# Optimization experiments

Measured on AMD Instinct MI355X. Metric: run time of the kernel, lower is better.

## Reference

```python
import jax, jax.numpy as jnp
import numpy as np

N_NODES = 50000
N_EDGES = 800000
MUL = 32            # multiplicity of 0e and 1o feature irreps
N_SPECIES = 4       # node_attr = 4x0e one-hot
N_BASIS = 8         # radial basis scalars
N_HID = 8           # invariant_neurons
AVG_NEIGH = 16.0
INV_SQRT3 = 1.0 / np.sqrt(3.0).astype(np.float32)


def setup_inputs() -> dict:
    key = jax.random.key(0)
    ks = jax.random.split(key, 16)
    x = jax.random.normal(ks[0], (N_NODES, MUL * 4), jnp.float32)  # 32x0e + 32x1o
    species = jax.random.randint(ks[1], (N_NODES,), 0, N_SPECIES)
    node_attr = jax.nn.one_hot(species, N_SPECIES, dtype=jnp.float32)
    edge_embedding = jax.random.normal(ks[2], (N_EDGES, N_BASIS), jnp.float32)
    edge_attr = jax.random.normal(ks[3], (N_EDGES, 4), jnp.float32)  # 1x0e + 1x1o
    edge_index = jax.random.randint(ks[4], (2, N_EDGES), 0, N_NODES)
    # learned params
    W_lin1_s = jax.random.normal(ks[5], (MUL, MUL), jnp.float32)
    W_lin1_v = jax.random.normal(ks[6], (MUL, MUL), jnp.float32)
    fc_w1 = jax.random.normal(ks[7], (N_BASIS, N_HID), jnp.float32)
    fc_w2 = jax.random.normal(ks[8], (N_HID, 4 * MUL), jnp.float32)  # tp.weight_numel = 4*MUL
    W_lin2_s = jax.random.normal(ks[9], (2 * MUL, MUL), jnp.float32)  # mid simplify: 64x0e
    W_lin2_v = jax.random.normal(ks[10], (2 * MUL, MUL), jnp.float32)  # 64x1o
    W_sc_s = jax.random.normal(ks[11], (MUL, N_SPECIES, MUL), jnp.float32)
    W_sc_v = jax.random.normal(ks[12], (MUL, N_SPECIES, MUL), jnp.float32)
    return dict(node_features=x, node_attr=node_attr, edge_embedding=edge_embedding,
                edge_attr=edge_attr, edge_index=edge_index,
                W_lin1_s=W_lin1_s, W_lin1_v=W_lin1_v, fc_w1=fc_w1, fc_w2=fc_w2,
                W_lin2_s=W_lin2_s, W_lin2_v=W_lin2_v, W_sc_s=W_sc_s, W_sc_v=W_sc_v)


def _forward(node_features, node_attr, edge_embedding, edge_attr, edge_index,
             W_lin1_s, W_lin1_v, fc_w1, fc_w2, W_lin2_s, W_lin2_v, W_sc_s, W_sc_v):
    n = node_features.shape[0]
    xs = node_features[:, :MUL]                       # [N, 32] scalars (0e)
    xv = node_features[:, MUL:].reshape(n, MUL, 3)    # [N, 32, 3] vectors (1o)

    # self-connection: FullyConnectedTensorProduct(feat, 4x0e -> feat), uvw weights
    sc_norm = 1.0 / np.sqrt(MUL * N_SPECIES).astype(np.float32)
    sc_s = jnp.einsum('nu,nv,uvw->nw', xs, node_attr, W_sc_s) * sc_norm
    sc_v = jnp.einsum('nui,nv,uvw->nwi', xv, node_attr, W_sc_v) * sc_norm

    # linear_1: per-irrep channel mixing, 1/sqrt(fan_in)
    l1n = 1.0 / np.sqrt(MUL).astype(np.float32)
    ys = (xs @ W_lin1_s) * l1n
    yv = jnp.einsum('nui,uw->nwi', xv, W_lin1_v) * l1n

    # radial MLP -> per-edge tensor-product weights (4 paths x MUL)
    h = jax.nn.silu((edge_embedding @ fc_w1) / np.sqrt(N_BASIS).astype(np.float32))
    w = (h @ fc_w2) / np.sqrt(N_HID).astype(np.float32)  # [E, 128]
    w00, w01, w10, w11 = jnp.split(w, 4, axis=1)          # instruction order (0,0),(0,1),(1,0),(1,1)

    src = edge_index[0]
    dst = edge_index[1]
    es = ys[src]                                          # [E, 32]
    ev = yv[src]                                          # [E, 32, 3]
    a0 = edge_attr[:, 0]                                  # [E]    0e
    a1 = edge_attr[:, 1:4]                                # [E, 3] 1o

    # per-edge weighted uvu tensor product paths
    o_s_a = w00 * es * a0[:, None]                                       # 0e x 0e -> 0e
    o_s_b = w11 * jnp.einsum('eui,ei->eu', ev, a1) * INV_SQRT3           # 1o x 1o -> 0e
    o_v_a = (w01 * es)[:, :, None] * a1[:, None, :]                      # 0e x 1o -> 1o
    o_v_b = w10[:, :, None] * ev * a0[:, None, None]                     # 1o x 0e -> 1o

    # scatter-sum to destination nodes
    mid_s = jax.ops.segment_sum(jnp.concatenate([o_s_a, o_s_b], axis=1), dst, num_segments=n)
    mid_v = jax.ops.segment_sum(jnp.concatenate([o_v_a, o_v_b], axis=1), dst, num_segments=n)
    inv = 1.0 / np.sqrt(AVG_NEIGH).astype(np.float32)
    mid_s = mid_s * inv   # [N, 64]
    mid_v = mid_v * inv   # [N, 64, 3]

    # linear_2: 64x0e+64x1o -> 32x0e+32x1o
    l2n = 1.0 / np.sqrt(2 * MUL).astype(np.float32)
    out_s = (mid_s @ W_lin2_s) * l2n + sc_s
    out_v = jnp.einsum('nui,uw->nwi', mid_v, W_lin2_v) * l2n + sc_v
    return jnp.concatenate([out_s, out_v.reshape(n, MUL * 3)], axis=1)


def reference(node_features, node_attr, edge_embedding, edge_attr, edge_index,
              W_lin1_s, W_lin1_v, fc_w1, fc_w2, W_lin2_s, W_lin2_v, W_sc_s, W_sc_v):
    return _forward(node_features, node_attr, edge_embedding, edge_attr, edge_index,
                    W_lin1_s, W_lin1_v, fc_w1, fc_w2, W_lin2_s, W_lin2_v, W_sc_s, W_sc_v)
```

## Files before the change

kernel.cpp:

```cpp
#include <hip/hip_runtime.h>
#include <hip/hip_bf16.h>

#define N_NODES 50000
#define N_EDGES 800000
#define CAP 64
#define NODE_BLOCKS (N_NODES / 8)
#define FILM_BLOCKS ((N_EDGES + 256) / 256)

__device__ __forceinline__ unsigned short f2bf(float f) {
    union { float f; unsigned u; } t; t.f = f;
    unsigned r = t.u + 0x7FFF + ((t.u >> 16) & 1);
    return (unsigned short)(r >> 16);
}

__global__ __launch_bounds__(256) void prep_kernel(
    const float* __restrict__ x, const float* __restrict__ attr,
    const float* __restrict__ W1s, const float* __restrict__ W1v,
    const float* __restrict__ Wscs, const float* __restrict__ Wscv,
    const float* __restrict__ ee, const float* __restrict__ eattr,
    const int* __restrict__ eidx, const float* __restrict__ fcw1,
    int* __restrict__ counts, int2* __restrict__ bucket,
    float* __restrict__ rec,
    unsigned short* __restrict__ ysvh, float* __restrict__ out)
{
    __shared__ float shm[11264];
    const int tid = threadIdx.x;

    if (blockIdx.x < NODE_BLOCKS) {
        const int node0 = blockIdx.x * 8;
        ((float4*)shm)[tid] = ((const float4*)(x + (long)node0 * 128))[tid];
        ((float4*)(shm + 1024))[tid] = ((const float4*)W1s)[tid];
        ((float4*)(shm + 2048))[tid] = ((const float4*)W1v)[tid];
        #pragma unroll
        for (int i = 0; i < 4; ++i) {
            ((float4*)(shm + 3072))[tid + i*256] = ((const float4*)Wscs)[tid + i*256];
            ((float4*)(shm + 7168))[tid + i*256] = ((const float4*)Wscv)[tid + i*256];
        }
        __syncthreads();

        const int nl = tid >> 5;
        const int w  = tid & 31;
        const int node = node0 + nl;

        const float* at = attr + (long)node * 4;
        int sp = 0;
        if (at[1] > 0.5f) sp = 1;
        if (at[2] > 0.5f) sp = 2;
        if (at[3] > 0.5f) sp = 3;

        const float* lx   = shm + nl * 128;
        const float* l1s  = shm + 1024;
        const float* l1v  = shm + 2048;
        const float* lscs = shm + 3072 + sp * 32;
        const float* lscv = shm + 7168 + sp * 32;

        float ys = 0.f, yv0 = 0.f, yv1 = 0.f, yv2 = 0.f;
        float ss = 0.f, sv0 = 0.f, sv1 = 0.f, sv2 = 0.f;
        #pragma unroll 8
        for (int u = 0; u < 32; ++u) {
            const float xs = lx[u];
            const float x0 = lx[32 + 3*u + 0];
            const float x1 = lx[32 + 3*u + 1];
            const float x2 = lx[32 + 3*u + 2];
            const float w1s = l1s[u*32 + w];
            const float w1v = l1v[u*32 + w];
            const float wss = lscs[u*128 + w];
            const float wsv = lscv[u*128 + w];
            ys  += xs * w1s;
            yv0 += x0 * w1v;  yv1 += x1 * w1v;  yv2 += x2 * w1v;
            ss  += xs * wss;
            sv0 += x0 * wsv;  sv1 += x1 * wsv;  sv2 += x2 * wsv;
        }
        const float l1n = 0.17677669529663687f;
        const float scn = 0.08838834764831843f;

        uint2 pk;
        pk.x = (unsigned)f2bf(ys  * l1n) | ((unsigned)f2bf(yv0 * l1n) << 16);
        pk.y = (unsigned)f2bf(yv1 * l1n) | ((unsigned)f2bf(yv2 * l1n) << 16);
        *(uint2*)(ysvh + (long)node * 128 + w * 4) = pk;

        float* op = out + (long)node * 128;
        op[w] = ss * scn;
        op[32 + 3*w + 0] = sv0 * scn;
        op[32 + 3*w + 1] = sv1 * scn;
        op[32 + 3*w + 2] = sv2 * scn;
    } else {
        if (tid < 64) shm[tid] = fcw1[tid];
        __syncthreads();

        const int e = (blockIdx.x - NODE_BLOCKS) * 256 + tid;
        if (e < N_EDGES) {
            const float4 ea = ((const float4*)(ee + (long)e * 8))[0];
            const float4 eb = ((const float4*)(ee + (long)e * 8))[1];
            const float eev[8] = {ea.x, ea.y, ea.z, ea.w, eb.x, eb.y, eb.z, eb.w};
            const float inv_sqrt8 = 0.35355339059327373f;
            float h[8];
            #pragma unroll
            for (int j = 0; j < 8; ++j) {
                float pre = 0.f;
                #pragma unroll
                for (int b = 0; b < 8; ++b) pre += eev[b] * shm[b*8 + j];
                pre *= inv_sqrt8;
                h[j] = pre / (1.f + __expf(-pre)) * inv_sqrt8;
            }
            float* rp = rec + (long)e * 12;
            ((float4*)rp)[0] = make_float4(h[0], h[1], h[2], h[3]);
            ((float4*)rp)[1] = make_float4(h[4], h[5], h[6], h[7]);
            ((float4*)rp)[2] = ((const float4*)eattr)[e];

            const int src = eidx[e];
            const int dst = eidx[N_EDGES + e];
            const int slot = atomicAdd(&counts[dst], 1);
            if (slot < CAP) bucket[(long)dst * CAP + slot] = make_int2(e, src);
        } else if (e == N_EDGES) {
            float* rp = rec + (long)e * 12;
            ((float4*)rp)[0] = make_float4(0.f, 0.f, 0.f, 0.f);
            ((float4*)rp)[1] = make_float4(0.f, 0.f, 0.f, 0.f);
            ((float4*)rp)[2] = make_float4(0.f, 0.f, 0.f, 0.f);
        }
    }
}

__global__ __launch_bounds__(256) void agg_kernel(
    const float* __restrict__ fcw2,
    const float* __restrict__ W2s, const float* __restrict__ W2v,
    const unsigned short* __restrict__ ysvh,
    const int* __restrict__ counts, const int2* __restrict__ bucket,
    const float* __restrict__ rec,
    float* __restrict__ out)
{
    __shared__ float mid[8][256];

    const int tid = threadIdx.x;
    const int nl = tid >> 5;
    const int u  = tid & 31;
    const int node = blockIdx.x * 8 + nl;

    float f2r[8][4];
    #pragma unroll
    for (int j = 0; j < 8; ++j) {
        f2r[j][0] = fcw2[j*128 + u];
        f2r[j][1] = fcw2[j*128 + 32 + u];
        f2r[j][2] = fcw2[j*128 + 64 + u];
        f2r[j][3] = fcw2[j*128 + 96 + u];
    }

    const int cnt = min(counts[node], CAP);
    int2 b0 = bucket[(long)node * CAP + u];
    if (u >= cnt) b0 = make_int2(N_EDGES, 0);

    float msa = 0.f, msb = 0.f;
    float va0 = 0.f, va1 = 0.f, va2 = 0.f;
    float vb0 = 0.f, vb1 = 0.f, vb2 = 0.f;

    #define ACCUM(HA, HB, AT, Y)                                             \
    {                                                                        \
        const float es = __uint_as_float((Y).x << 16);                       \
        const float ex = __uint_as_float((Y).x & 0xffff0000u);               \
        const float ey = __uint_as_float((Y).y << 16);                       \
        const float ez = __uint_as_float((Y).y & 0xffff0000u);               \
        const float hh[8] = {HA.x,HA.y,HA.z,HA.w,HB.x,HB.y,HB.z,HB.w};       \
        float w00=0.f, w01=0.f, w10=0.f, w11=0.f;                            \
        _Pragma("unroll")                                                    \
        for (int j = 0; j < 8; ++j) {                                        \
            w00 += hh[j]*f2r[j][0]; w01 += hh[j]*f2r[j][1];                  \
            w10 += hh[j]*f2r[j][2]; w11 += hh[j]*f2r[j][3];                  \
        }                                                                    \
        const float a0 = AT.x, a1x = AT.y, a1y = AT.z, a1z = AT.w;           \
        msa += w00 * es * a0;                                                \
        msb += w11 * (ex*a1x + ey*a1y + ez*a1z);                             \
        const float t = w01 * es;                                            \
        va0 += t*a1x; va1 += t*a1y; va2 += t*a1z;                            \
        const float s = w10 * a0;                                            \
        vb0 += s*ex; vb1 += s*ey; vb2 += s*ez;                               \
    }

    #define FETCH(K, RA0,RB0,RT0, RA1,RB1,RT1, Y0,Y1)                        \
    {                                                                        \
        const int fe0 = __shfl(b0.x, (K),     32);                           \
        const int fs0 = __shfl(b0.y, (K),     32);                           \
        const int fe1 = __shfl(b0.x, (K) + 1, 32);                           \
        const int fs1 = __shfl(b0.y, (K) + 1, 32);                           \
        const float4* r0p = (const float4*)(rec + (long)fe0 * 12);           \
        const float4* r1p = (const float4*)(rec + (long)fe1 * 12);           \
        RA0 = r0p[0]; RB0 = r0p[1]; RT0 = r0p[2];                            \
        RA1 = r1p[0]; RB1 = r1p[1]; RT1 = r1p[2];                            \
        Y0 = *(const uint2*)(ysvh + (long)fs0 * 128 + u * 4);                \
        Y1 = *(const uint2*)(ysvh + (long)fs1 * 128 + u * 4);                \
    }

    const int c0 = min(cnt, 32);
    float4 cA0, cB0, cT0, cA1, cB1, cT1; uint2 cy0, cy1;
    FETCH(0, cA0,cB0,cT0, cA1,cB1,cT1, cy0, cy1)
    for (int k = 0; k < c0; k += 2) {
        float4 nA0, nB0, nT0, nA1, nB1, nT1; uint2 ny0, ny1;
        FETCH((k + 2) & 31, nA0,nB0,nT0, nA1,nB1,nT1, ny0, ny1)
        ACCUM(cA0, cB0, cT0, cy0)
        ACCUM(cA1, cB1, cT1, cy1)
        cA0=nA0; cB0=nB0; cT0=nT0; cA1=nA1; cB1=nB1; cT1=nT1; cy0=ny0; cy1=ny1;
    }

    if (cnt > 32) {
        int2 b1 = bucket[(long)node * CAP + 32 + u];
        if (32 + u >= cnt) b1 = make_int2(N_EDGES, 0);
        for (int k = 0; k < cnt - 32; k += 2) {
            const int e0 = __shfl(b1.x, k, 32),     s0 = __shfl(b1.y, k, 32);
            const int e1 = __shfl(b1.x, k + 1, 32), s1 = __shfl(b1.y, k + 1, 32);
            const float4* r0p = (const float4*)(rec + (long)e0 * 12);
            const float4* r1p = (const float4*)(rec + (long)e1 * 12);
            const float4 A0 = r0p[0], B0 = r0p[1], T0 = r0p[2];
            const float4 A1 = r1p[0], B1 = r1p[1], T1 = r1p[2];
            const uint2 y0 = *(const uint2*)(ysvh + (long)s0 * 128 + u * 4);
            const uint2 y1 = *(const uint2*)(ysvh + (long)s1 * 128 + u * 4);
            ACCUM(A0, B0, T0, y0)
            ACCUM(A1, B1, T1, y1)
        }
    }
    #undef FETCH
    #undef ACCUM

    msb *= 0.5773502691896258f;

    float* m = mid[nl];
    m[u]       = msa;
    m[32 + u]  = msb;
    m[64  + u*3 + 0] = va0;  m[64  + u*3 + 1] = va1;  m[64  + u*3 + 2] = va2;
    m[160 + u*3 + 0] = vb0;  m[160 + u*3 + 1] = vb1;  m[160 + u*3 + 2] = vb2;
    __syncthreads();

    float os = 0.f, ov0 = 0.f, ov1 = 0.f, ov2 = 0.f;
    #pragma unroll 8
    for (int q = 0; q < 32; ++q) {
        const float wsa = W2s[q*32 + u];
        const float wsb = W2s[(32 + q)*32 + u];
        os += m[q] * wsa + m[32 + q] * wsb;
        const float wva = W2v[q*32 + u];
        const float wvb = W2v[(32 + q)*32 + u];
        ov0 += m[64 + q*3 + 0] * wva + m[160 + q*3 + 0] * wvb;
        ov1 += m[64 + q*3 + 1] * wva + m[160 + q*3 + 1] * wvb;
        ov2 += m[64 + q*3 + 2] * wva + m[160 + q*3 + 2] * wvb;
    }

    const float sc = 0.03125f;
    float* op = out + (long)node * 128;
    op[u]            += os  * sc;
    op[32 + 3*u + 0] += ov0 * sc;
    op[32 + 3*u + 1] += ov1 * sc;
    op[32 + 3*u + 2] += ov2 * sc;
}

extern "C" void kernel_launch(void* const* d_in, const int* in_sizes, int n_in,
                              void* d_out, int out_size, void* d_ws, size_t ws_size,
                              hipStream_t stream) {
    const float* x     = (const float*)d_in[0];
    const float* attr  = (const float*)d_in[1];
    const float* ee    = (const float*)d_in[2];
    const float* eattr = (const float*)d_in[3];
    const int*   eidx  = (const int*)  d_in[4];
    const float* W1s   = (const float*)d_in[5];
    const float* W1v   = (const float*)d_in[6];
    const float* fcw1  = (const float*)d_in[7];
    const float* fcw2  = (const float*)d_in[8];
    const float* W2s   = (const float*)d_in[9];
    const float* W2v   = (const float*)d_in[10];
    const float* Wscs  = (const float*)d_in[11];
    const float* Wscv  = (const float*)d_in[12];

    float* out = (float*)d_out;

    unsigned short* ysvh = (unsigned short*)d_ws;
    int*   counts = (int*)(ysvh + (long)N_NODES * 128);
    int2*  bucket = (int2*)(counts + N_NODES);
    float* rec    = (float*)(bucket + (long)N_NODES * CAP);

    hipMemsetAsync(counts, 0, N_NODES * sizeof(int), stream);
    prep_kernel<<<NODE_BLOCKS + FILM_BLOCKS, 256, 0, stream>>>(
        x, attr, W1s, W1v, Wscs, Wscv, ee, eattr, eidx, fcw1,
        counts, bucket, rec, ysvh, out);
    agg_kernel<<<N_NODES/8, 256, 0, stream>>>(fcw2, W2s, W2v, ysvh,
                                              counts, bucket, rec, out);
}
```

Before: 292.1 us.

## Use 64-lane wave per node in aggregation and batch nodes per prep block

The prep kernel now has each block handle 40 nodes in 5 batches, so the ~40KB of shared weights is loaded once per block instead of once per 8 nodes. The aggregation kernel gives each node a full 64-lane wavefront, with the two halves processing alternating edges and then combining results with xor shuffles. The per-node linear_2 step now broadcasts values with shuffles instead of going through shared memory, and the W2 weights are staged in shared memory. This trades fewer nodes per block and an extra reduction for more parallel edge gathers per node and no mid-buffer barrier.

After: 321.1 us. +9.9%, slower.

```diff
diff --git a/kernel.cpp b/kernel.cpp
--- a/kernel.cpp
+++ b/kernel.cpp
@@ -4,7 +4,7 @@
 #define N_NODES 50000
 #define N_EDGES 800000
 #define CAP 64
-#define NODE_BLOCKS (N_NODES / 8)
+#define NODE_GS_BLOCKS 1250
 #define FILM_BLOCKS ((N_EDGES + 256) / 256)
 
 __device__ __forceinline__ unsigned short f2bf(float f) {
@@ -26,9 +26,7 @@
     __shared__ float shm[11264];
     const int tid = threadIdx.x;
 
-    if (blockIdx.x < NODE_BLOCKS) {
-        const int node0 = blockIdx.x * 8;
-        ((float4*)shm)[tid] = ((const float4*)(x + (long)node0 * 128))[tid];
+    if (blockIdx.x < NODE_GS_BLOCKS) {
         ((float4*)(shm + 1024))[tid] = ((const float4*)W1s)[tid];
         ((float4*)(shm + 2048))[tid] = ((const float4*)W1v)[tid];
         #pragma unroll
@@ -36,59 +34,65 @@
             ((float4*)(shm + 3072))[tid + i*256] = ((const float4*)Wscs)[tid + i*256];
             ((float4*)(shm + 7168))[tid + i*256] = ((const float4*)Wscv)[tid + i*256];
         }
-        __syncthreads();
 
         const int nl = tid >> 5;
         const int w  = tid & 31;
-        const int node = node0 + nl;
-
-        const float* at = attr + (long)node * 4;
-        int sp = 0;
-        if (at[1] > 0.5f) sp = 1;
-        if (at[2] > 0.5f) sp = 2;
-        if (at[3] > 0.5f) sp = 3;
-
-        const float* lx   = shm + nl * 128;
-        const float* l1s  = shm + 1024;
-        const float* l1v  = shm + 2048;
-        const float* lscs = shm + 3072 + sp * 32;
-        const float* lscv = shm + 7168 + sp * 32;
-
-        float ys = 0.f, yv0 = 0.f, yv1 = 0.f, yv2 = 0.f;
-        float ss = 0.f, sv0 = 0.f, sv1 = 0.f, sv2 = 0.f;
-        #pragma unroll 8
-        for (int u = 0; u < 32; ++u) {
-            const float xs = lx[u];
-            const float x0 = lx[32 + 3*u + 0];
-            const float x1 = lx[32 + 3*u + 1];
-            const float x2 = lx[32 + 3*u + 2];
-            const float w1s = l1s[u*32 + w];
-            const float w1v = l1v[u*32 + w];
-            const float wss = lscs[u*128 + w];
-            const float wsv = lscv[u*128 + w];
-            ys  += xs * w1s;
-            yv0 += x0 * w1v;  yv1 += x1 * w1v;  yv2 += x2 * w1v;
-            ss  += xs * wss;
-            sv0 += x0 * wsv;  sv1 += x1 * wsv;  sv2 += x2 * wsv;
-        }
         const float l1n = 0.17677669529663687f;
         const float scn = 0.08838834764831843f;
 
-        uint2 pk;
-        pk.x = (unsigned)f2bf(ys  * l1n) | ((unsigned)f2bf(yv0 * l1n) << 16);
-        pk.y = (unsigned)f2bf(yv1 * l1n) | ((unsigned)f2bf(yv2 * l1n) << 16);
-        *(uint2*)(ysvh + (long)node * 128 + w * 4) = pk;
-
-        float* op = out + (long)node * 128;
-        op[w] = ss * scn;
-        op[32 + 3*w + 0] = sv0 * scn;
-        op[32 + 3*w + 1] = sv1 * scn;
-        op[32 + 3*w + 2] = sv2 * scn;
+        for (int batch = 0; batch < 5; ++batch) {
+            const int node0 = blockIdx.x * 40 + batch * 8;
+            __syncthreads();
+            ((float4*)shm)[tid] = ((const float4*)(x + (long)node0 * 128))[tid];
+            __syncthreads();
+
+            const int node = node0 + nl;
+            const float* at = attr + (long)node * 4;
+            int sp = 0;
+            if (at[1] > 0.5f) sp = 1;
+            if (at[2] > 0.5f) sp = 2;
+            if (at[3] > 0.5f) sp = 3;
+
+            const float* lx   = shm + nl * 128;
+            const float* l1s  = shm + 1024;
+            const float* l1v  = shm + 2048;
+            const float* lscs = shm + 3072 + sp * 32;
+            const float* lscv = shm + 7168 + sp * 32;
+
+            float ys = 0.f, yv0 = 0.f, yv1 = 0.f, yv2 = 0.f;
+            float ss = 0.f, sv0 = 0.f, sv1 = 0.f, sv2 = 0.f;
+            #pragma unroll 8
+            for (int u = 0; u < 32; ++u) {
+                const float xs = lx[u];
+                const float x0 = lx[32 + 3*u + 0];
+                const float x1 = lx[32 + 3*u + 1];
+                const float x2 = lx[32 + 3*u + 2];
+                const float w1s = l1s[u*32 + w];
+                const float w1v = l1v[u*32 + w];
+                const float wss = lscs[u*128 + w];
+                const float wsv = lscv[u*128 + w];
+                ys  += xs * w1s;
+                yv0 += x0 * w1v;  yv1 += x1 * w1v;  yv2 += x2 * w1v;
+                ss  += xs * wss;
+                sv0 += x0 * wsv;  sv1 += x1 * wsv;  sv2 += x2 * wsv;
+            }
+
+            uint2 pk;
+            pk.x = (unsigned)f2bf(ys  * l1n) | ((unsigned)f2bf(yv0 * l1n) << 16);
+            pk.y = (unsigned)f2bf(yv1 * l1n) | ((unsigned)f2bf(yv2 * l1n) << 16);
+            *(uint2*)(ysvh + (long)node * 128 + w * 4) = pk;
+
+            float* op = out + (long)node * 128;
+            op[w] = ss * scn;
+            op[32 + 3*w + 0] = sv0 * scn;
+            op[32 + 3*w + 1] = sv1 * scn;
+            op[32 + 3*w + 2] = sv2 * scn;
+        }
     } else {
         if (tid < 64) shm[tid] = fcw1[tid];
         __syncthreads();
 
-        const int e = (blockIdx.x - NODE_BLOCKS) * 256 + tid;
+        const int e = (blockIdx.x - NODE_GS_BLOCKS) * 256 + tid;
         if (e < N_EDGES) {
             const float4 ea = ((const float4*)(ee + (long)e * 8))[0];
             const float4 eb = ((const float4*)(ee + (long)e * 8))[1];
@@ -129,12 +133,18 @@
     const float* __restrict__ rec,
     float* __restrict__ out)
 {
-    __shared__ float mid[8][256];
+    __shared__ float w2s[2048];
+    __shared__ float w2v[2048];
 
     const int tid = threadIdx.x;
-    const int nl = tid >> 5;
-    const int u  = tid & 31;
-    const int node = blockIdx.x * 8 + nl;
+    for (int i = tid; i < 2048; i += 256) { w2s[i] = W2s[i]; w2v[i] = W2v[i]; }
+    __syncthreads();
+
+    const int nl   = tid >> 6;
+    const int lane = tid & 63;
+    const int u    = lane & 31;
+    const int half = lane >> 5;
+    const int node = blockIdx.x * 4 + nl;
 
     float f2r[8][4];
     #pragma unroll
@@ -146,8 +156,8 @@
     }
 
     const int cnt = min(counts[node], CAP);
-    int2 b0 = bucket[(long)node * CAP + u];
-    if (u >= cnt) b0 = make_int2(N_EDGES, 0);
+    int2 b = bucket[(long)node * CAP + lane];
+    if (lane >= cnt) b = make_int2(N_EDGES, 0);
 
     float msa = 0.f, msb = 0.f;
     float va0 = 0.f, va1 = 0.f, va2 = 0.f;
@@ -175,78 +185,61 @@
         vb0 += s*ex; vb1 += s*ey; vb2 += s*ez;                               \
     }
 
-    #define FETCH(K, RA0,RB0,RT0, RA1,RB1,RT1, Y0,Y1)                        \
+    #define FETCH(SLOT, RA, RB, RT, Y)                                       \
     {                                                                        \
-        const int fe0 = __shfl(b0.x, (K),     32);                           \
-        const int fs0 = __shfl(b0.y, (K),     32);                           \
-        const int fe1 = __shfl(b0.x, (K) + 1, 32);                           \
-        const int fs1 = __shfl(b0.y, (K) + 1, 32);                           \
-        const float4* r0p = (const float4*)(rec + (long)fe0 * 12);           \
-        const float4* r1p = (const float4*)(rec + (long)fe1 * 12);           \
-        RA0 = r0p[0]; RB0 = r0p[1]; RT0 = r0p[2];                            \
-        RA1 = r1p[0]; RB1 = r1p[1]; RT1 = r1p[2];                            \
-        Y0 = *(const uint2*)(ysvh + (long)fs0 * 128 + u * 4);                \
-        Y1 = *(const uint2*)(ysvh + (long)fs1 * 128 + u * 4);                \
-    }
-
-    const int c0 = min(cnt, 32);
-    float4 cA0, cB0, cT0, cA1, cB1, cT1; uint2 cy0, cy1;
-    FETCH(0, cA0,cB0,cT0, cA1,cB1,cT1, cy0, cy1)
-    for (int k = 0; k < c0; k += 2) {
-        float4 nA0, nB0, nT0, nA1, nB1, nT1; uint2 ny0, ny1;
-        FETCH((k + 2) & 31, nA0,nB0,nT0, nA1,nB1,nT1, ny0, ny1)
-        ACCUM(cA0, cB0, cT0, cy0)
-        ACCUM(cA1, cB1, cT1, cy1)
-        cA0=nA0; cB0=nB0; cT0=nT0; cA1=nA1; cB1=nB1; cT1=nT1; cy0=ny0; cy1=ny1;
-    }
-
-    if (cnt > 32) {
-        int2 b1 = bucket[(long)node * CAP + 32 + u];
-        if (32 + u >= cnt) b1 = make_int2(N_EDGES, 0);
-        for (int k = 0; k < cnt - 32; k += 2) {
-            const int e0 = __shfl(b1.x, k, 32),     s0 = __shfl(b1.y, k, 32);
-            const int e1 = __shfl(b1.x, k + 1, 32), s1 = __shfl(b1.y, k + 1, 32);
-            const float4* r0p = (const float4*)(rec + (long)e0 * 12);
-            const float4* r1p = (const float4*)(rec + (long)e1 * 12);
-            const float4 A0 = r0p[0], B0 = r0p[1], T0 = r0p[2];
-            const float4 A1 = r1p[0], B1 = r1p[1], T1 = r1p[2];
-            const uint2 y0 = *(const uint2*)(ysvh + (long)s0 * 128 + u * 4);
-            const uint2 y1 = *(const uint2*)(ysvh + (long)s1 * 128 + u * 4);
-            ACCUM(A0, B0, T0, y0)
-            ACCUM(A1, B1, T1, y1)
-        }
+        const int fe = __shfl(b.x, (SLOT), 64);                              \
+        const int fs = __shfl(b.y, (SLOT), 64);                              \
+        const float4* rp = (const float4*)(rec + (long)fe * 12);             \
+        RA = rp[0]; RB = rp[1]; RT = rp[2];                                  \
+        Y = *(const uint2*)(ysvh + (long)fs * 128 + u * 4);                  \
+    }
+
+    float4 cA, cB, cT; uint2 cy;
+    FETCH(half, cA, cB, cT, cy)
+    for (int k = 0; k < cnt; k += 2) {
+        float4 nA, nB, nT; uint2 ny;
+        int ns = k + 2 + half;
+        if (ns > 63) ns = 63;
+        FETCH(ns, nA, nB, nT, ny)
+        ACCUM(cA, cB, cT, cy)
+        cA = nA; cB = nB; cT = nT; cy = ny;
     }
     #undef FETCH
     #undef ACCUM
 
+    msa += __shfl_xor(msa, 32, 64);
+    msb += __shfl_xor(msb, 32, 64);
+    va0 += __shfl_xor(va0, 32, 64);
+    va1 += __shfl_xor(va1, 32, 64);
+    va2 += __shfl_xor(va2, 32, 64);
+    vb0 += __shfl_xor(vb0, 32, 64);
+    vb1 += __shfl_xor(vb1, 32, 64);
+    vb2 += __shfl_xor(vb2, 32, 64);
     msb *= 0.5773502691896258f;
 
-    float* m = mid[nl];
-    m[u]       = msa;
-    m[32 + u]  = msb;
-    m[64  + u*3 + 0] = va0;  m[64  + u*3 + 1] = va1;  m[64  + u*3 + 2] = va2;
-    m[160 + u*3 + 0] = vb0;  m[160 + u*3 + 1] = vb1;  m[160 + u*3 + 2] = vb2;
-    __syncthreads();
-
-    float os = 0.f, ov0 = 0.f, ov1 = 0.f, ov2 = 0.f;
+    const float  pA = half ? va1 : msa;
+    const float  pB = half ? vb1 : msb;
+    const float  pC = half ? va2 : va0;
+    const float  pD = half ? vb2 : vb0;
+    const float* WA = half ? w2v : w2s;
+
+    float A = 0.f, B = 0.f;
     #pragma unroll 8
     for (int q = 0; q < 32; ++q) {
-        const float wsa = W2s[q*32 + u];
-        const float wsb = W2s[(32 + q)*32 + u];
-        os += m[q] * wsa + m[32 + q] * wsb;
-        const float wva = W2v[q*32 + u];
-        const float wvb = W2v[(32 + q)*32 + u];
-        ov0 += m[64 + q*3 + 0] * wva + m[160 + q*3 + 0] * wvb;
-        ov1 += m[64 + q*3 + 1] * wva + m[160 + q*3 + 1] * wvb;
-        ov2 += m[64 + q*3 + 2] * wva + m[160 + q*3 + 2] * wvb;
+        const float aq = __shfl(pA, q, 32);
+        const float bq = __shfl(pB, q, 32);
+        const float cq = __shfl(pC, q, 32);
+        const float dq = __shfl(pD, q, 32);
+        A += aq * WA[q*32 + u]  + bq * WA[(32 + q)*32 + u];
+        B += cq * w2v[q*32 + u] + dq * w2v[(32 + q)*32 + u];
     }
 
     const float sc = 0.03125f;
     float* op = out + (long)node * 128;
-    op[u]            += os  * sc;
-    op[32 + 3*u + 0] += ov0 * sc;
-    op[32 + 3*u + 1] += ov1 * sc;
-    op[32 + 3*u + 2] += ov2 * sc;
+    const int ia = half ? (32 + 3*u + 1) : u;
+    const int ib = half ? (32 + 3*u + 2) : (32 + 3*u + 0);
+    op[ia] += A * sc;
+    op[ib] += B * sc;
 }
 
 extern "C" void kernel_launch(void* const* d_in, const int* in_sizes, int n_in,
@@ -274,9 +267,9 @@
     float* rec    = (float*)(bucket + (long)N_NODES * CAP);
 
     hipMemsetAsync(counts, 0, N_NODES * sizeof(int), stream);
-    prep_kernel<<<NODE_BLOCKS + FILM_BLOCKS, 256, 0, stream>>>(
+    prep_kernel<<<NODE_GS_BLOCKS + FILM_BLOCKS, 256, 0, stream>>>(
         x, attr, W1s, W1v, Wscs, Wscv, ee, eattr, eidx, fcw1,
         counts, bucket, rec, ysvh, out);
-    agg_kernel<<<N_NODES/8, 256, 0, stream>>>(fcw2, W2s, W2v, ysvh,
+    agg_kernel<<<N_NODES/4, 256, 0, stream>>>(fcw2, W2s, W2v, ysvh,
                                               counts, bucket, rec, out);
 }
```

## Move edge radial MLP into aggregation kernel and batch node blocks

Applied to the files above, without the earlier changes.

The per-edge radial MLP (fc_w1 + SiLU) and the edge_attr load move out of the prep kernel into the aggregation kernel. Each lane computes the hidden vector for its own bucketed edge and stores it in LDS, which removes the 12-float per-edge record write and its later gather from global memory. Node blocks in the prep kernel now process 5 batches of 8 nodes each, so the weight matrices are loaded into shared memory fewer times. Edges past 32 per node recompute the MLP inline for each edge. The __syncthreads before the linear_2 stage is removed; this appears safe because each node's wavefront only reads its own mid row, which relies on 32-lane groups staying within one wavefront.

After: 285.7 us. 1.02x faster.

```diff
diff --git a/kernel.cpp b/kernel.cpp
--- a/kernel.cpp
+++ b/kernel.cpp
@@ -4,8 +4,8 @@
 #define N_NODES 50000
 #define N_EDGES 800000
 #define CAP 64
-#define NODE_BLOCKS (N_NODES / 8)
-#define FILM_BLOCKS ((N_EDGES + 256) / 256)
+#define NODE_GS_BLOCKS 1250
+#define BUCKET_BLOCKS (N_EDGES/256)
 
 __device__ __forceinline__ unsigned short f2bf(float f) {
     union { float f; unsigned u; } t; t.f = f;
@@ -17,18 +17,14 @@
     const float* __restrict__ x, const float* __restrict__ attr,
     const float* __restrict__ W1s, const float* __restrict__ W1v,
     const float* __restrict__ Wscs, const float* __restrict__ Wscv,
-    const float* __restrict__ ee, const float* __restrict__ eattr,
-    const int* __restrict__ eidx, const float* __restrict__ fcw1,
+    const int* __restrict__ eidx,
     int* __restrict__ counts, int2* __restrict__ bucket,
-    float* __restrict__ rec,
     unsigned short* __restrict__ ysvh, float* __restrict__ out)
 {
     __shared__ float shm[11264];
     const int tid = threadIdx.x;
 
-    if (blockIdx.x < NODE_BLOCKS) {
-        const int node0 = blockIdx.x * 8;
-        ((float4*)shm)[tid] = ((const float4*)(x + (long)node0 * 128))[tid];
+    if (blockIdx.x < NODE_GS_BLOCKS) {
         ((float4*)(shm + 1024))[tid] = ((const float4*)W1s)[tid];
         ((float4*)(shm + 2048))[tid] = ((const float4*)W1v)[tid];
         #pragma unroll
@@ -36,105 +32,85 @@
             ((float4*)(shm + 3072))[tid + i*256] = ((const float4*)Wscs)[tid + i*256];
             ((float4*)(shm + 7168))[tid + i*256] = ((const float4*)Wscv)[tid + i*256];
         }
-        __syncthreads();
 
         const int nl = tid >> 5;
         const int w  = tid & 31;
-        const int node = node0 + nl;
-
-        const float* at = attr + (long)node * 4;
-        int sp = 0;
-        if (at[1] > 0.5f) sp = 1;
-        if (at[2] > 0.5f) sp = 2;
-        if (at[3] > 0.5f) sp = 3;
-
-        const float* lx   = shm + nl * 128;
-        const float* l1s  = shm + 1024;
-        const float* l1v  = shm + 2048;
-        const float* lscs = shm + 3072 + sp * 32;
-        const float* lscv = shm + 7168 + sp * 32;
-
-        float ys = 0.f, yv0 = 0.f, yv1 = 0.f, yv2 = 0.f;
-        float ss = 0.f, sv0 = 0.f, sv1 = 0.f, sv2 = 0.f;
-        #pragma unroll 8
-        for (int u = 0; u < 32; ++u) {
-            const float xs = lx[u];
-            const float x0 = lx[32 + 3*u + 0];
-            const float x1 = lx[32 + 3*u + 1];
-            const float x2 = lx[32 + 3*u + 2];
-            const float w1s = l1s[u*32 + w];
-            const float w1v = l1v[u*32 + w];
-            const float wss = lscs[u*128 + w];
-            const float wsv = lscv[u*128 + w];
-            ys  += xs * w1s;
-            yv0 += x0 * w1v;  yv1 += x1 * w1v;  yv2 += x2 * w1v;
-            ss  += xs * wss;
-            sv0 += x0 * wsv;  sv1 += x1 * wsv;  sv2 += x2 * wsv;
-        }
         const float l1n = 0.17677669529663687f;
         const float scn = 0.08838834764831843f;
 
-        uint2 pk;
-        pk.x = (unsigned)f2bf(ys  * l1n) | ((unsigned)f2bf(yv0 * l1n) << 16);
-        pk.y = (unsigned)f2bf(yv1 * l1n) | ((unsigned)f2bf(yv2 * l1n) << 16);
-        *(uint2*)(ysvh + (long)node * 128 + w * 4) = pk;
-
-        float* op = out + (long)node * 128;
-        op[w] = ss * scn;
-        op[32 + 3*w + 0] = sv0 * scn;
-        op[32 + 3*w + 1] = sv1 * scn;
-        op[32 + 3*w + 2] = sv2 * scn;
+        for (int batch = 0; batch < 5; ++batch) {
+            const int node0 = blockIdx.x * 40 + batch * 8;
+            __syncthreads();
+            ((float4*)shm)[tid] = ((const float4*)(x + (long)node0 * 128))[tid];
+            __syncthreads();
+
+            const int node = node0 + nl;
+            const float* at = attr + (long)node * 4;
+            int sp = 0;
+            if (at[1] > 0.5f) sp = 1;
+            if (at[2] > 0.5f) sp = 2;
+            if (at[3] > 0.5f) sp = 3;
+
+            const float* lx   = shm + nl * 128;
+            const float* l1s  = shm + 1024;
+            const float* l1v  = shm + 2048;
+            const float* lscs = shm + 3072 + sp * 32;
+            const float* lscv = shm + 7168 + sp * 32;
+
+            float ys = 0.f, yv0 = 0.f, yv1 = 0.f, yv2 = 0.f;
+            float ss = 0.f, sv0 = 0.f, sv1 = 0.f, sv2 = 0.f;
+            #pragma unroll 8
+            for (int u = 0; u < 32; ++u) {
+                const float xs = lx[u];
+                const float x0 = lx[32 + 3*u + 0];
+                const float x1 = lx[32 + 3*u + 1];
+                const float x2 = lx[32 + 3*u + 2];
+                const float w1s = l1s[u*32 + w];
+                const float w1v = l1v[u*32 + w];
+                const float wss = lscs[u*128 + w];
+                const float wsv = lscv[u*128 + w];
+                ys  += xs * w1s;
+                yv0 += x0 * w1v;  yv1 += x1 * w1v;  yv2 += x2 * w1v;
+                ss  += xs * wss;
+                sv0 += x0 * wsv;  sv1 += x1 * wsv;  sv2 += x2 * wsv;
+            }
+
+            uint2 pk;
+            pk.x = (unsigned)f2bf(ys  * l1n) | ((unsigned)f2bf(yv0 * l1n) << 16);
+            pk.y = (unsigned)f2bf(yv1 * l1n) | ((unsigned)f2bf(yv2 * l1n) << 16);
+            *(uint2*)(ysvh + (long)node * 128 + w * 4) = pk;
+
+            float* op = out + (long)node * 128;
+            op[w] = ss * scn;
+            op[32 + 3*w + 0] = sv0 * scn;
+            op[32 + 3*w + 1] = sv1 * scn;
+            op[32 + 3*w + 2] = sv2 * scn;
+        }
     } else {
-        if (tid < 64) shm[tid] = fcw1[tid];
-        __syncthreads();
-
-        const int e = (blockIdx.x - NODE_BLOCKS) * 256 + tid;
-        if (e < N_EDGES) {
-            const float4 ea = ((const float4*)(ee + (long)e * 8))[0];
-            const float4 eb = ((const float4*)(ee + (long)e * 8))[1];
-            const float eev[8] = {ea.x, ea.y, ea.z, ea.w, eb.x, eb.y, eb.z, eb.w};
-            const float inv_sqrt8 = 0.35355339059327373f;
-            float h[8];
-            #pragma unroll
-            for (int j = 0; j < 8; ++j) {
-                float pre = 0.f;
-                #pragma unroll
-                for (int b = 0; b < 8; ++b) pre += eev[b] * shm[b*8 + j];
-                pre *= inv_sqrt8;
-                h[j] = pre / (1.f + __expf(-pre)) * inv_sqrt8;
-            }
-            float* rp = rec + (long)e * 12;
-            ((float4*)rp)[0] = make_float4(h[0], h[1], h[2], h[3]);
-            ((float4*)rp)[1] = make_float4(h[4], h[5], h[6], h[7]);
-            ((float4*)rp)[2] = ((const float4*)eattr)[e];
-
-            const int src = eidx[e];
-            const int dst = eidx[N_EDGES + e];
-            const int slot = atomicAdd(&counts[dst], 1);
-            if (slot < CAP) bucket[(long)dst * CAP + slot] = make_int2(e, src);
-        } else if (e == N_EDGES) {
-            float* rp = rec + (long)e * 12;
-            ((float4*)rp)[0] = make_float4(0.f, 0.f, 0.f, 0.f);
-            ((float4*)rp)[1] = make_float4(0.f, 0.f, 0.f, 0.f);
-            ((float4*)rp)[2] = make_float4(0.f, 0.f, 0.f, 0.f);
-        }
+        const int e = (blockIdx.x - NODE_GS_BLOCKS) * 256 + tid;
+        const int src = eidx[e];
+        const int dst = eidx[N_EDGES + e];
+        const int slot = atomicAdd(&counts[dst], 1);
+        if (slot < CAP) bucket[(long)dst * CAP + slot] = make_int2(e, src);
     }
 }
 
 __global__ __launch_bounds__(256) void agg_kernel(
-    const float* __restrict__ fcw2,
+    const float* __restrict__ ee, const float* __restrict__ eattr,
+    const float* __restrict__ fcw1, const float* __restrict__ fcw2,
     const float* __restrict__ W2s, const float* __restrict__ W2v,
     const unsigned short* __restrict__ ysvh,
     const int* __restrict__ counts, const int2* __restrict__ bucket,
-    const float* __restrict__ rec,
     float* __restrict__ out)
 {
+    __shared__ float hrec[8][32 * 12];
     __shared__ float mid[8][256];
 
     const int tid = threadIdx.x;
     const int nl = tid >> 5;
     const int u  = tid & 31;
     const int node = blockIdx.x * 8 + nl;
+    const float inv_sqrt8 = 0.35355339059327373f;
 
     float f2r[8][4];
     #pragma unroll
@@ -147,7 +123,29 @@
 
     const int cnt = min(counts[node], CAP);
     int2 b0 = bucket[(long)node * CAP + u];
-    if (u >= cnt) b0 = make_int2(N_EDGES, 0);
+    const bool dummy = (u >= cnt);
+    if (dummy) b0 = make_int2(0, 0);
+
+    {
+        const float4 ea = ((const float4*)(ee + (long)b0.x * 8))[0];
+        const float4 eb = ((const float4*)(ee + (long)b0.x * 8))[1];
+        const float4 at = ((const float4*)eattr)[b0.x];
+        const float eev[8] = {ea.x, ea.y, ea.z, ea.w, eb.x, eb.y, eb.z, eb.w};
+        float* hr = hrec[nl] + u * 12;
+        float h[8];
+        #pragma unroll
+        for (int j = 0; j < 8; ++j) {
+            float pre = 0.f;
+            #pragma unroll
+            for (int b = 0; b < 8; ++b) pre += eev[b] * fcw1[b*8 + j];
+            pre *= inv_sqrt8;
+            const float s = pre / (1.f + __expf(-pre)) * inv_sqrt8;
+            h[j] = dummy ? 0.f : s;
+        }
+        ((float4*)hr)[0] = make_float4(h[0], h[1], h[2], h[3]);
+        ((float4*)hr)[1] = make_float4(h[4], h[5], h[6], h[7]);
+        ((float4*)hr)[2] = at;
+    }
 
     float msa = 0.f, msb = 0.f;
     float va0 = 0.f, va1 = 0.f, va2 = 0.f;
@@ -175,48 +173,53 @@
         vb0 += s*ex; vb1 += s*ey; vb2 += s*ez;                               \
     }
 
-    #define FETCH(K, RA0,RB0,RT0, RA1,RB1,RT1, Y0,Y1)                        \
-    {                                                                        \
-        const int fe0 = __shfl(b0.x, (K),     32);                           \
-        const int fs0 = __shfl(b0.y, (K),     32);                           \
-        const int fe1 = __shfl(b0.x, (K) + 1, 32);                           \
-        const int fs1 = __shfl(b0.y, (K) + 1, 32);                           \
-        const float4* r0p = (const float4*)(rec + (long)fe0 * 12);           \
-        const float4* r1p = (const float4*)(rec + (long)fe1 * 12);           \
-        RA0 = r0p[0]; RB0 = r0p[1]; RT0 = r0p[2];                            \
-        RA1 = r1p[0]; RB1 = r1p[1]; RT1 = r1p[2];                            \
-        Y0 = *(const uint2*)(ysvh + (long)fs0 * 128 + u * 4);                \
-        Y1 = *(const uint2*)(ysvh + (long)fs1 * 128 + u * 4);                \
-    }
-
     const int c0 = min(cnt, 32);
-    float4 cA0, cB0, cT0, cA1, cB1, cT1; uint2 cy0, cy1;
-    FETCH(0, cA0,cB0,cT0, cA1,cB1,cT1, cy0, cy1)
-    for (int k = 0; k < c0; k += 2) {
-        float4 nA0, nB0, nT0, nA1, nB1, nT1; uint2 ny0, ny1;
-        FETCH((k + 2) & 31, nA0,nB0,nT0, nA1,nB1,nT1, ny0, ny1)
-        ACCUM(cA0, cB0, cT0, cy0)
-        ACCUM(cA1, cB1, cT1, cy1)
-        cA0=nA0; cB0=nB0; cT0=nT0; cA1=nA1; cB1=nB1; cT1=nT1; cy0=ny0; cy1=ny1;
+    {
+        int s0 = __shfl(b0.y, 0, 32);
+        int s1 = __shfl(b0.y, 1, 32);
+        uint2 y0 = *(const uint2*)(ysvh + (long)s0 * 128 + u * 4);
+        uint2 y1 = *(const uint2*)(ysvh + (long)s1 * 128 + u * 4);
+        for (int k = 0; k < c0; k += 2) {
+            const int kn = (k + 2) & 31;
+            const int sn0 = __shfl(b0.y, kn, 32);
+            const int sn1 = __shfl(b0.y, kn + 1, 32);
+            uint2 yn0 = *(const uint2*)(ysvh + (long)sn0 * 128 + u * 4);
+            uint2 yn1 = *(const uint2*)(ysvh + (long)sn1 * 128 + u * 4);
+            const float4* h0p = (const float4*)(hrec[nl] + k * 12);
+            const float4* h1p = (const float4*)(hrec[nl] + (k + 1) * 12);
+            const float4 A0 = h0p[0], B0 = h0p[1], T0 = h0p[2];
+            const float4 A1 = h1p[0], B1 = h1p[1], T1 = h1p[2];
+            ACCUM(A0, B0, T0, y0)
+            ACCUM(A1, B1, T1, y1)
+            y0 = yn0; y1 = yn1;
+        }
     }
 
     if (cnt > 32) {
         int2 b1 = bucket[(long)node * CAP + 32 + u];
-        if (32 + u >= cnt) b1 = make_int2(N_EDGES, 0);
-        for (int k = 0; k < cnt - 32; k += 2) {
-            const int e0 = __shfl(b1.x, k, 32),     s0 = __shfl(b1.y, k, 32);
-            const int e1 = __shfl(b1.x, k + 1, 32), s1 = __shfl(b1.y, k + 1, 32);
-            const float4* r0p = (const float4*)(rec + (long)e0 * 12);
-            const float4* r1p = (const float4*)(rec + (long)e1 * 12);
-            const float4 A0 = r0p[0], B0 = r0p[1], T0 = r0p[2];
-            const float4 A1 = r1p[0], B1 = r1p[1], T1 = r1p[2];
-            const uint2 y0 = *(const uint2*)(ysvh + (long)s0 * 128 + u * 4);
-            const uint2 y1 = *(const uint2*)(ysvh + (long)s1 * 128 + u * 4);
-            ACCUM(A0, B0, T0, y0)
-            ACCUM(A1, B1, T1, y1)
-        }
-    }
-    #undef FETCH
+        for (int k = 32; k < cnt; ++k) {
+            const int e = __shfl(b1.x, k - 32, 32);
+            const int s = __shfl(b1.y, k - 32, 32);
+            const float4 ea = ((const float4*)(ee + (long)e * 8))[0];
+            const float4 eb = ((const float4*)(ee + (long)e * 8))[1];
+            const float4 at = ((const float4*)eattr)[e];
+            const float eev[8] = {ea.x, ea.y, ea.z, ea.w, eb.x, eb.y, eb.z, eb.w};
+            float4 HA, HB;
+            float h[8];
+            #pragma unroll
+            for (int j = 0; j < 8; ++j) {
+                float pre = 0.f;
+                #pragma unroll
+                for (int b = 0; b < 8; ++b) pre += eev[b] * fcw1[b*8 + j];
+                pre *= inv_sqrt8;
+                h[j] = pre / (1.f + __expf(-pre)) * inv_sqrt8;
+            }
+            HA = make_float4(h[0], h[1], h[2], h[3]);
+            HB = make_float4(h[4], h[5], h[6], h[7]);
+            const uint2 y = *(const uint2*)(ysvh + (long)s * 128 + u * 4);
+            ACCUM(HA, HB, at, y)
+        }
+    }
     #undef ACCUM
 
     msb *= 0.5773502691896258f;
@@ -226,7 +229,6 @@
     m[32 + u]  = msb;
     m[64  + u*3 + 0] = va0;  m[64  + u*3 + 1] = va1;  m[64  + u*3 + 2] = va2;
     m[160 + u*3 + 0] = vb0;  m[160 + u*3 + 1] = vb1;  m[160 + u*3 + 2] = vb2;
-    __syncthreads();
 
     float os = 0.f, ov0 = 0.f, ov1 = 0.f, ov2 = 0.f;
     #pragma unroll 8
@@ -271,12 +273,10 @@
     unsigned short* ysvh = (unsigned short*)d_ws;
     int*   counts = (int*)(ysvh + (long)N_NODES * 128);
     int2*  bucket = (int2*)(counts + N_NODES);
-    float* rec    = (float*)(bucket + (long)N_NODES * CAP);
 
     hipMemsetAsync(counts, 0, N_NODES * sizeof(int), stream);
-    prep_kernel<<<NODE_BLOCKS + FILM_BLOCKS, 256, 0, stream>>>(
-        x, attr, W1s, W1v, Wscs, Wscv, ee, eattr, eidx, fcw1,
-        counts, bucket, rec, ysvh, out);
-    agg_kernel<<<N_NODES/8, 256, 0, stream>>>(fcw2, W2s, W2v, ysvh,
-                                              counts, bucket, rec, out);
-}
+    prep_kernel<<<NODE_GS_BLOCKS + BUCKET_BLOCKS, 256, 0, stream>>>(
+        x, attr, W1s, W1v, Wscs, Wscv, eidx, counts, bucket, ysvh, out);
+    agg_kernel<<<N_NODES/8, 256, 0, stream>>>(ee, eattr, fcw1, fcw2, W2s, W2v,
+                                              ysvh, counts, bucket, out);
+}
```
